# Kernel optimization log

Measured on AMD Instinct MI355X. Metric: run time of the kernel, lower is better.

Reference implementation:

```python
import jax, jax.numpy as jnp
import numpy as np

N = 50000
E = 800000
D = 64
EPS_BN = 1e-5
EPS_NORM = 1e-12


def _bn_train(x, gamma, beta):
    # BatchNorm1d in training mode: batch stats over axis 0, biased variance
    mu = jnp.mean(x, axis=0, keepdims=True)
    var = jnp.mean((x - mu) ** 2, axis=0, keepdims=True)
    return (x - mu) / jnp.sqrt(var + EPS_BN) * gamma + beta


def setup_inputs() -> dict:
    key = jax.random.key(0)
    ks = jax.random.split(key, 16)
    s = 1.0 / np.sqrt(D)
    s2 = 1.0 / np.sqrt(2 * D)
    return {
        "h": jax.random.normal(ks[0], (N, D), jnp.float32),
        "e": jax.random.normal(ks[1], (E, D), jnp.float32),
        "src": jax.random.randint(ks[2], (E,), 0, N, jnp.int32),
        "dst": jax.random.randint(ks[3], (E,), 0, N, jnp.int32),
        "A_W": jax.random.uniform(ks[4], (D, D), jnp.float32, -s, s),
        "A_b": jax.random.uniform(ks[5], (D,), jnp.float32, -s, s),
        "B_W": jax.random.uniform(ks[6], (D, D), jnp.float32, -s, s),
        "B_b": jax.random.uniform(ks[7], (D,), jnp.float32, -s, s),
        "C_W": jax.random.uniform(ks[8], (D, D), jnp.float32, -s, s),
        "C_b": jax.random.uniform(ks[9], (D,), jnp.float32, -s, s),
        "W_apply": jax.random.uniform(ks[10], (2 * D, D), jnp.float32, -s2, s2),
        "b_apply": jax.random.uniform(ks[11], (D,), jnp.float32, -s2, s2),
        "gamma_h": jnp.ones((D,), jnp.float32),
        "beta_h": jnp.zeros((D,), jnp.float32),
        "gamma_e": jnp.ones((D,), jnp.float32),
        "beta_e": jnp.zeros((D,), jnp.float32),
    }


def reference(h, e, src, dst, A_W, A_b, B_W, B_b, C_W, C_b,
              W_apply, b_apply, gamma_h, beta_h, gamma_e, beta_e):
    h_in, e_in = h, e
    # dropout p=0 -> identity
    Ah = h @ A_W + A_b            # [N, D]
    Bh = h @ B_W + B_b            # [N, D]
    Ce = e @ C_W + C_b            # [E, D]

    # message: e_ij = Ce + Bh_src + Bh_dst ; gated message sigma(e_ij)*Ah_src
    e_ij = Ce + Bh[src] + Bh[dst]                 # [E, D]
    msg = jax.nn.relu(jax.nn.sigmoid(e_ij) * Ah[src])  # [E, D]

    # reduce: per-destination-node max over mailbox
    c = jax.ops.segment_max(msg, dst, num_segments=N)  # [N, D], -inf if empty
    deg = jax.ops.segment_sum(jnp.ones((E,), msg.dtype), dst, num_segments=N)
    c = jnp.where(deg[:, None] > 0, c, 0.0)

    # apply/update: concat -> linear -> L2 normalize -> activation
    bundle = jnp.concatenate([h, c], axis=1) @ W_apply + b_apply  # [N, D]
    norm = jnp.sqrt(jnp.sum(bundle * bundle, axis=1, keepdims=True))
    bundle = bundle / jnp.maximum(norm, EPS_NORM)
    h_new = jax.nn.relu(bundle)

    e_new = jax.nn.relu(e_ij)

    h_new = _bn_train(h_new, gamma_h, beta_h)
    e_new = _bn_train(e_new, gamma_e, beta_e)

    h_out = h_in + h_new
    e_out = e_in + e_new
    return (h_out, e_out)
```

## Files before the change

kernel.cpp:

```cpp
#include <hip/hip_runtime.h>

typedef __attribute__((ext_vector_type(8))) short short8;
typedef __attribute__((ext_vector_type(4))) float f32x4;
typedef __attribute__((ext_vector_type(4))) unsigned short u16x4;
typedef __attribute__((ext_vector_type(4))) unsigned int u32x4;

#define DEV static __device__ __forceinline__

constexpr int NN = 50000;
constexpr int NE = 800000;
constexpr int NT_N = NN / 16;
constexpr int NT_E = NE / 16;
constexpr float EPS_BN = 1e-5f;
constexpr float EPS_NORM = 1e-12f;

DEV unsigned short f2b(float f) {
  unsigned u = __float_as_uint(f);
  return (unsigned short)((u + 0x7FFFu + ((u >> 16) & 1u)) >> 16);
}
DEV float b2f(unsigned short s) { return __uint_as_float(((unsigned)s) << 16); }

DEV short8 load_a_frag(const float* __restrict__ base, int row, int kbase) {
  const f32x4* p = reinterpret_cast<const f32x4*>(base + row * 64 + kbase);
  f32x4 v0 = p[0], v1 = p[1];
  short8 a;
  a[0] = f2b(v0[0]); a[1] = f2b(v0[1]); a[2] = f2b(v0[2]); a[3] = f2b(v0[3]);
  a[4] = f2b(v1[0]); a[5] = f2b(v1[1]); a[6] = f2b(v1[2]); a[7] = f2b(v1[3]);
  return a;
}

DEV short8 load_w_frag(const float* __restrict__ W, int kbase, int c0, int lane) {
  int kr = kbase + ((lane >> 4) << 3);
  int cc = c0 + (lane & 15);
  short8 b;
#pragma unroll
  for (int j = 0; j < 8; ++j) b[j] = f2b(W[(kr + j) * 64 + cc]);
  return b;
}

DEV f32x4 mfma16(short8 a, short8 b, f32x4 c) {
  return __builtin_amdgcn_mfma_f32_16x16x32_bf16(a, b, c, 0, 0, 0);
}

__global__ void k_init(u32x4* __restrict__ cbuf4, float* __restrict__ stats) {
  int i = blockIdx.x * 256 + threadIdx.x;
  if (i < NN * 16) {
    u32x4 z = {0u, 0u, 0u, 0u};
    cbuf4[i] = z;
  }
  if (i < 256) stats[i] = 0.0f;
}

__global__ void __launch_bounds__(256) k_node_lin(
    const float* __restrict__ h, const float* __restrict__ AW,
    const float* __restrict__ Ab, const float* __restrict__ BW,
    const float* __restrict__ Bb, float* __restrict__ Ah,
    float* __restrict__ Bh) {
  int lane = threadIdx.x & 63, warp = threadIdx.x >> 6;
  int tile = blockIdx.x * 4 + warp;
  if (tile >= NT_N) return;

  short8 wa[4][2], wb[4][2];
  float ab[4], bb[4];
#pragma unroll
  for (int t = 0; t < 4; ++t) {
#pragma unroll
    for (int kk = 0; kk < 2; ++kk) {
      wa[t][kk] = load_w_frag(AW, kk * 32, t * 16, lane);
      wb[t][kk] = load_w_frag(BW, kk * 32, t * 16, lane);
    }
    ab[t] = Ab[t * 16 + (lane & 15)];
    bb[t] = Bb[t * 16 + (lane & 15)];
  }

  int row0 = tile * 16;
  int ar = row0 + (lane & 15), kb = (lane >> 4) * 8;
  short8 a0 = load_a_frag(h, ar, kb);
  short8 a1 = load_a_frag(h, ar, 32 + kb);

  f32x4 zero = {0.f, 0.f, 0.f, 0.f};
  f32x4 accA[4], accB[4];
#pragma unroll
  for (int t = 0; t < 4; ++t) {
    accA[t] = mfma16(a0, wa[t][0], zero);
    accA[t] = mfma16(a1, wa[t][1], accA[t]);
    accB[t] = mfma16(a0, wb[t][0], zero);
    accB[t] = mfma16(a1, wb[t][1], accB[t]);
  }
#pragma unroll
  for (int t = 0; t < 4; ++t)
#pragma unroll
    for (int q = 0; q < 4; ++q) {
      int row = row0 + (lane >> 4) * 4 + q;
      int col = t * 16 + (lane & 15);
      Ah[row * 64 + col] = accA[t][q] + ab[t];
      Bh[row * 64 + col] = accB[t][q] + bb[t];
    }
}

__global__ void __launch_bounds__(256) k_edge(
    const float* __restrict__ e, const int* __restrict__ src,
    const int* __restrict__ dst, const float* __restrict__ CW,
    const float* __restrict__ Cb, const float* __restrict__ Ah,
    const float* __restrict__ Bh, unsigned* __restrict__ cbuf,
    float* __restrict__ gsum, float* __restrict__ gsq,
    float* __restrict__ stage_f32, unsigned short* __restrict__ stage_b16,
    int use_b16) {
  __shared__ float ssum[64], ssq[64];
  int lane = threadIdx.x & 63, warp = threadIdx.x >> 6;

  short8 cw[4][2];
  float cb[4];
#pragma unroll
  for (int t = 0; t < 4; ++t) {
#pragma unroll
    for (int kk = 0; kk < 2; ++kk) cw[t][kk] = load_w_frag(CW, kk * 32, t * 16, lane);
    cb[t] = Cb[t * 16 + (lane & 15)];
  }

  float es[4] = {0.f, 0.f, 0.f, 0.f}, eq[4] = {0.f, 0.f, 0.f, 0.f};
  f32x4 zero = {0.f, 0.f, 0.f, 0.f};
  int stride = gridDim.x * 4;

  for (int tile = blockIdx.x * 4 + warp; tile < NT_E; tile += stride) {
    int e0 = tile * 16;
    int ar = e0 + (lane & 15), kb = (lane >> 4) * 8;
    short8 a0 = load_a_frag(e, ar, kb);
    short8 a1 = load_a_frag(e, ar, 32 + kb);

    f32x4 acc[4];
#pragma unroll
    for (int t = 0; t < 4; ++t) {
      acc[t] = mfma16(a0, cw[t][0], zero);
      acc[t] = mfma16(a1, cw[t][1], acc[t]);
    }

#pragma unroll
    for (int q = 0; q < 4; ++q) {
      int er = e0 + (lane >> 4) * 4 + q;
      int s = src[er], d = dst[er];
#pragma unroll
      for (int t = 0; t < 4; ++t) {
        int col = t * 16 + (lane & 15);
        float eij = acc[t][q] + cb[t] + Bh[s * 64 + col] + Bh[d * 64 + col];
        float sg = __fdividef(1.0f, 1.0f + __expf(-eij));
        float m = sg * Ah[s * 64 + col];
        m = (m > 0.0f) ? m : 0.0f;
        atomicMax(&cbuf[d * 64 + col], __float_as_uint(m));
        float re = (eij > 0.0f) ? eij : 0.0f;
        if (use_b16) stage_b16[er * 64 + col] = f2b(re);
        else         stage_f32[er * 64 + col] = re;
        es[t] += re;
        eq[t] += re * re;
      }
    }
  }

  if (threadIdx.x < 64) { ssum[threadIdx.x] = 0.f; ssq[threadIdx.x] = 0.f; }
  __syncthreads();
#pragma unroll
  for (int t = 0; t < 4; ++t) {
    int col = t * 16 + (lane & 15);
    atomicAdd(&ssum[col], es[t]);
    atomicAdd(&ssq[col], eq[t]);
  }
  __syncthreads();
  if (threadIdx.x < 64) {
    atomicAdd(&gsum[threadIdx.x], ssum[threadIdx.x]);
    atomicAdd(&gsq[threadIdx.x], ssq[threadIdx.x]);
  }
}

__global__ void __launch_bounds__(256) k_apply(
    const float* __restrict__ h, const float* __restrict__ cbuf_f,
    const float* __restrict__ Wap, const float* __restrict__ bap,
    float* __restrict__ stage_h, float* __restrict__ gsum,
    float* __restrict__ gsq) {
  __shared__ float ssum[64], ssq[64];
  int lane = threadIdx.x & 63, warp = threadIdx.x >> 6;
  int tile = blockIdx.x * 4 + warp;

  float hs[4] = {0.f, 0.f, 0.f, 0.f}, hq[4] = {0.f, 0.f, 0.f, 0.f};

  if (tile < NT_N) {
    short8 w[4][4];
    float ba[4];
#pragma unroll
    for (int t = 0; t < 4; ++t) {
#pragma unroll
      for (int kk = 0; kk < 4; ++kk) w[t][kk] = load_w_frag(Wap, kk * 32, t * 16, lane);
      ba[t] = bap[t * 16 + (lane & 15)];
    }

    int row0 = tile * 16;
    int ar = row0 + (lane & 15), kb = (lane >> 4) * 8;
    short8 a0 = load_a_frag(h, ar, kb);
    short8 a1 = load_a_frag(h, ar, 32 + kb);
    short8 a2 = load_a_frag(cbuf_f, ar, kb);
    short8 a3 = load_a_frag(cbuf_f, ar, 32 + kb);

    f32x4 zero = {0.f, 0.f, 0.f, 0.f};
    f32x4 acc[4];
#pragma unroll
    for (int t = 0; t < 4; ++t) {
      acc[t] = mfma16(a0, w[t][0], zero);
      acc[t] = mfma16(a1, w[t][1], acc[t]);
      acc[t] = mfma16(a2, w[t][2], acc[t]);
      acc[t] = mfma16(a3, w[t][3], acc[t]);
    }

    float v[4][4];
#pragma unroll
    for (int t = 0; t < 4; ++t)
#pragma unroll
      for (int q = 0; q < 4; ++q) v[t][q] = acc[t][q] + ba[t];

#pragma unroll
    for (int q = 0; q < 4; ++q) {
      float sq = v[0][q] * v[0][q] + v[1][q] * v[1][q] + v[2][q] * v[2][q] +
                 v[3][q] * v[3][q];
      sq += __shfl_xor(sq, 1);
      sq += __shfl_xor(sq, 2);
      sq += __shfl_xor(sq, 4);
      sq += __shfl_xor(sq, 8);
      float sc = __fdividef(1.0f, fmaxf(sqrtf(sq), EPS_NORM));
      int row = row0 + (lane >> 4) * 4 + q;
#pragma unroll
      for (int t = 0; t < 4; ++t) {
        float hn = v[t][q] * sc;
        hn = (hn > 0.0f) ? hn : 0.0f;
        stage_h[row * 64 + t * 16 + (lane & 15)] = hn;
        hs[t] += hn;
        hq[t] += hn * hn;
      }
    }
  }

  if (threadIdx.x < 64) { ssum[threadIdx.x] = 0.f; ssq[threadIdx.x] = 0.f; }
  __syncthreads();
#pragma unroll
  for (int t = 0; t < 4; ++t) {
    int col = t * 16 + (lane & 15);
    atomicAdd(&ssum[col], hs[t]);
    atomicAdd(&ssq[col], hq[t]);
  }
  __syncthreads();
  if (threadIdx.x < 64) {
    atomicAdd(&gsum[threadIdx.x], ssum[threadIdx.x]);
    atomicAdd(&gsq[threadIdx.x], ssq[threadIdx.x]);
  }
}

__global__ void k_stats(const float* __restrict__ sum_e, const float* __restrict__ sq_e,
                        const float* __restrict__ sum_h, const float* __restrict__ sq_h,
                        const float* __restrict__ gamma_e, const float* __restrict__ beta_e,
                        const float* __restrict__ gamma_h, const float* __restrict__ beta_h,
                        float* __restrict__ se, float* __restrict__ oe,
                        float* __restrict__ sh, float* __restrict__ oh) {
  int j = threadIdx.x;
  if (j < 64) {
    float mu = sum_e[j] / (float)NE;
    float var = fmaxf(sq_e[j] / (float)NE - mu * mu, 0.0f);
    float s = gamma_e[j] / sqrtf(var + EPS_BN);
    se[j] = s;
    oe[j] = beta_e[j] - mu * s;
    mu = sum_h[j] / (float)NN;
    var = fmaxf(sq_h[j] / (float)NN - mu * mu, 0.0f);
    s = gamma_h[j] / sqrtf(var + EPS_BN);
    sh[j] = s;
    oh[j] = beta_h[j] - mu * s;
  }
}

__global__ void __launch_bounds__(256) k_fin_h(const float* __restrict__ h,
                                               const float* __restrict__ sh,
                                               const float* __restrict__ oh,
                                               float* __restrict__ outh) {
  int i = (blockIdx.x * 256 + threadIdx.x) * 4;
  if (i >= NN * 64) return;
  f32x4 x = *reinterpret_cast<const f32x4*>(outh + i);
  f32x4 hv = *reinterpret_cast<const f32x4*>(h + i);
  int c0 = i & 63;
  f32x4 r;
#pragma unroll
  for (int j = 0; j < 4; ++j) r[j] = hv[j] + x[j] * sh[c0 + j] + oh[c0 + j];
  *reinterpret_cast<f32x4*>(outh + i) = r;
}

__global__ void __launch_bounds__(256) k_fin_e(const float* __restrict__ e,
                                               const float* __restrict__ se,
                                               const float* __restrict__ oe,
                                               const unsigned short* __restrict__ stb,
                                               int use_b16,
                                               float* __restrict__ oute) {
  int i = (blockIdx.x * 256 + threadIdx.x) * 4;
  if (i >= NE * 64) return;
  f32x4 x;
  if (use_b16) {
    u16x4 u = *reinterpret_cast<const u16x4*>(stb + i);
    x[0] = b2f(u[0]); x[1] = b2f(u[1]); x[2] = b2f(u[2]); x[3] = b2f(u[3]);
  } else {
    x = *reinterpret_cast<const f32x4*>(oute + i);
  }
  f32x4 ev = *reinterpret_cast<const f32x4*>(e + i);
  int c0 = i & 63;
  f32x4 r;
#pragma unroll
  for (int j = 0; j < 4; ++j) r[j] = ev[j] + x[j] * se[c0 + j] + oe[c0 + j];
  *reinterpret_cast<f32x4*>(oute + i) = r;
}

extern "C" void kernel_launch(void* const* d_in, const int* in_sizes, int n_in,
                              void* d_out, int out_size, void* d_ws, size_t ws_size,
                              hipStream_t stream) {
  (void)in_sizes; (void)n_in; (void)out_size;
  const float* h   = (const float*)d_in[0];
  const float* e   = (const float*)d_in[1];
  const int*   src = (const int*)d_in[2];
  const int*   dst = (const int*)d_in[3];
  const float* AW  = (const float*)d_in[4];
  const float* Ab  = (const float*)d_in[5];
  const float* BW  = (const float*)d_in[6];
  const float* Bb  = (const float*)d_in[7];
  const float* CW  = (const float*)d_in[8];
  const float* Cb  = (const float*)d_in[9];
  const float* Wap = (const float*)d_in[10];
  const float* bap = (const float*)d_in[11];
  const float* gamma_h = (const float*)d_in[12];
  const float* beta_h  = (const float*)d_in[13];
  const float* gamma_e = (const float*)d_in[14];
  const float* beta_e  = (const float*)d_in[15];

  float* ws = (float*)d_ws;
  float* Ah = ws;
  float* Bh = ws + 3200000;
  unsigned* cbuf = (unsigned*)(ws + 6400000);
  float* stats = ws + 9600000;
  float* sum_e = stats;
  float* sq_e  = stats + 64;
  float* sum_h = stats + 128;
  float* sq_h  = stats + 192;
  float* se    = stats + 256;
  float* oe    = stats + 320;
  float* sh    = stats + 384;
  float* oh    = stats + 448;

  size_t base_bytes = (size_t)(9600000 + 512) * 4;
  int use_b16 = (ws_size >= base_bytes + (size_t)NE * 64 * 2) ? 1 : 0;
  unsigned short* stage_b16 = (unsigned short*)(ws + 9600512);

  float* outh = (float*)d_out;
  float* oute = outh + (size_t)NN * 64;
  float* stage_f32 = oute;

  k_init<<<3125, 256, 0, stream>>>((u32x4*)cbuf, stats);
  k_node_lin<<<(NT_N + 3) / 4, 256, 0, stream>>>(h, AW, Ab, BW, Bb, Ah, Bh);
  k_edge<<<2048, 256, 0, stream>>>(e, src, dst, CW, Cb, Ah, Bh, cbuf, sum_e,
                                   sq_e, stage_f32, stage_b16, use_b16);
  k_apply<<<(NT_N + 3) / 4, 256, 0, stream>>>(h, (const float*)cbuf, Wap, bap,
                                              outh, sum_h, sq_h);
  k_stats<<<1, 64, 0, stream>>>(sum_e, sq_e, sum_h, sq_h, gamma_e, beta_e,
                                gamma_h, beta_h, se, oe, sh, oh);
  k_fin_h<<<NN * 64 / 1024, 256, 0, stream>>>(h, sh, oh, outh);
  k_fin_e<<<NE * 64 / 1024, 256, 0, stream>>>(e, se, oe, stage_b16, use_b16, oute);
}
```

Before: 392.9 us.

## Replace atomicMax segment-max with CSR-sorted per-node gather reduction

Builds a CSR grouping of edges by destination on each call (degree count, scan, scatter into perm) and replaces the per-element global atomicMax in the edge kernel with a separate per-node warp reduction. The edge kernel now stages pre-ReLU e_ij, and the reduce kernel recomputes sigmoid times Ah[src] from it. The final edge kernel applies the ReLU instead. This removes 51M contended atomics and the cbuf zeroing. In exchange it adds several small launches, an extra gather pass over the staged e_ij (bf16 or f32), and a nondeterministic perm order that does not affect a max.

```diff
diff --git a/kernel.cpp b/kernel.cpp
--- a/kernel.cpp
+++ b/kernel.cpp
@@ -3,7 +3,6 @@
 typedef __attribute__((ext_vector_type(8))) short short8;
 typedef __attribute__((ext_vector_type(4))) float f32x4;
 typedef __attribute__((ext_vector_type(4))) unsigned short u16x4;
-typedef __attribute__((ext_vector_type(4))) unsigned int u32x4;
 
 #define DEV static __device__ __forceinline__
 
@@ -11,6 +10,7 @@
 constexpr int NE = 800000;
 constexpr int NT_N = NN / 16;
 constexpr int NT_E = NE / 16;
+constexpr int NB_SCAN = (NN + 255) / 256;
 constexpr float EPS_BN = 1e-5f;
 constexpr float EPS_NORM = 1e-12f;
 
@@ -42,13 +42,67 @@
   return __builtin_amdgcn_mfma_f32_16x16x32_bf16(a, b, c, 0, 0, 0);
 }
 
-__global__ void k_init(u32x4* __restrict__ cbuf4, float* __restrict__ stats) {
+__global__ void k_init(int* __restrict__ deg, float* __restrict__ stats) {
   int i = blockIdx.x * 256 + threadIdx.x;
-  if (i < NN * 16) {
-    u32x4 z = {0u, 0u, 0u, 0u};
-    cbuf4[i] = z;
-  }
-  if (i < 256) stats[i] = 0.0f;
+  if (i < NN) deg[i] = 0;
+  if (i < 512) stats[i] = 0.0f;
+}
+
+__global__ void k_deg(const int* __restrict__ dst, int* __restrict__ deg) {
+  int i = blockIdx.x * 256 + threadIdx.x;
+  if (i < NE) atomicAdd(&deg[dst[i]], 1);
+}
+
+__global__ void k_scan_local(const int* __restrict__ deg, int* __restrict__ off,
+                             int* __restrict__ bsum) {
+  __shared__ int sh[256];
+  int t = threadIdx.x;
+  int i = blockIdx.x * 256 + t;
+  int v = (i < NN) ? deg[i] : 0;
+  sh[t] = v;
+  __syncthreads();
+  for (int s = 1; s < 256; s <<= 1) {
+    int u = (t >= s) ? sh[t - s] : 0;
+    __syncthreads();
+    sh[t] += u;
+    __syncthreads();
+  }
+  if (i < NN) off[i] = sh[t] - v;
+  if (t == 255) bsum[blockIdx.x] = sh[255];
+}
+
+__global__ void k_scan_base(const int* __restrict__ bsum, int* __restrict__ bbase) {
+  __shared__ int sh[256];
+  int t = threadIdx.x;
+  int v = (t < NB_SCAN) ? bsum[t] : 0;
+  sh[t] = v;
+  __syncthreads();
+  for (int s = 1; s < 256; s <<= 1) {
+    int u = (t >= s) ? sh[t - s] : 0;
+    __syncthreads();
+    sh[t] += u;
+    __syncthreads();
+  }
+  if (t < NB_SCAN) bbase[t] = sh[t] - v;
+}
+
+__global__ void k_scan_fix(const int* __restrict__ bbase, int* __restrict__ off,
+                           int* __restrict__ cursor) {
+  int i = blockIdx.x * 256 + threadIdx.x;
+  if (i < NN) {
+    int o = off[i] + bbase[blockIdx.x];
+    off[i] = o;
+    cursor[i] = o;
+  }
+}
+
+__global__ void k_scatter(const int* __restrict__ dst, int* __restrict__ cursor,
+                          int* __restrict__ perm) {
+  int i = blockIdx.x * 256 + threadIdx.x;
+  if (i < NE) {
+    int p = atomicAdd(&cursor[dst[i]], 1);
+    perm[p] = i;
+  }
 }
 
 __global__ void __launch_bounds__(256) k_node_lin(
@@ -101,8 +155,7 @@
 __global__ void __launch_bounds__(256) k_edge(
     const float* __restrict__ e, const int* __restrict__ src,
     const int* __restrict__ dst, const float* __restrict__ CW,
-    const float* __restrict__ Cb, const float* __restrict__ Ah,
-    const float* __restrict__ Bh, unsigned* __restrict__ cbuf,
+    const float* __restrict__ Cb, const float* __restrict__ Bh,
     float* __restrict__ gsum, float* __restrict__ gsq,
     float* __restrict__ stage_f32, unsigned short* __restrict__ stage_b16,
     int use_b16) {
@@ -143,13 +196,9 @@
       for (int t = 0; t < 4; ++t) {
         int col = t * 16 + (lane & 15);
         float eij = acc[t][q] + cb[t] + Bh[s * 64 + col] + Bh[d * 64 + col];
-        float sg = __fdividef(1.0f, 1.0f + __expf(-eij));
-        float m = sg * Ah[s * 64 + col];
-        m = (m > 0.0f) ? m : 0.0f;
-        atomicMax(&cbuf[d * 64 + col], __float_as_uint(m));
+        if (use_b16) stage_b16[er * 64 + col] = f2b(eij);
+        else         stage_f32[er * 64 + col] = eij;
         float re = (eij > 0.0f) ? eij : 0.0f;
-        if (use_b16) stage_b16[er * 64 + col] = f2b(re);
-        else         stage_f32[er * 64 + col] = re;
         es[t] += re;
         eq[t] += re * re;
       }
@@ -169,6 +218,36 @@
     atomicAdd(&gsum[threadIdx.x], ssum[threadIdx.x]);
     atomicAdd(&gsq[threadIdx.x], ssq[threadIdx.x]);
   }
+}
+
+__global__ void __launch_bounds__(256) k_reduce(
+    const int* __restrict__ deg, const int* __restrict__ off,
+    const int* __restrict__ perm, const int* __restrict__ src,
+    const float* __restrict__ Ah, const unsigned short* __restrict__ st16,
+    const float* __restrict__ stF, int use_b16, float* __restrict__ cbuf) {
+  int lane = threadIdx.x & 63, warp = threadIdx.x >> 6;
+  int node = blockIdx.x * 4 + warp;
+  if (node >= NN) return;
+  int cnt = deg[node], base = off[node];
+  float m = 0.0f;
+  for (int b0 = 0; b0 < cnt; b0 += 64) {
+    int nb = min(64, cnt - b0);
+    int eid = 0, s = 0;
+    if (lane < nb) {
+      eid = perm[base + b0 + lane];
+      s = src[eid];
+    }
+#pragma unroll 4
+    for (int j = 0; j < nb; ++j) {
+      int ej = __shfl(eid, j);
+      int sj = __shfl(s, j);
+      float x = use_b16 ? b2f(st16[ej * 64 + lane]) : stF[ej * 64 + lane];
+      float sg = __fdividef(1.0f, 1.0f + __expf(-x));
+      float mm = sg * Ah[sj * 64 + lane];
+      m = fmaxf(m, (mm > 0.0f) ? mm : 0.0f);
+    }
+  }
+  cbuf[node * 64 + lane] = m;
 }
 
 __global__ void __launch_bounds__(256) k_apply(
@@ -306,7 +385,10 @@
   int c0 = i & 63;
   f32x4 r;
 #pragma unroll
-  for (int j = 0; j < 4; ++j) r[j] = ev[j] + x[j] * se[c0 + j] + oe[c0 + j];
+  for (int j = 0; j < 4; ++j) {
+    float rx = (x[j] > 0.0f) ? x[j] : 0.0f;
+    r[j] = ev[j] + rx * se[c0 + j] + oe[c0 + j];
+  }
   *reinterpret_cast<f32x4*>(oute + i) = r;
 }
 
@@ -332,10 +414,9 @@
   const float* beta_e  = (const float*)d_in[15];
 
   float* ws = (float*)d_ws;
-  float* Ah = ws;
-  float* Bh = ws + 3200000;
-  unsigned* cbuf = (unsigned*)(ws + 6400000);
-  float* stats = ws + 9600000;
+  float* Ah  = ws;
+  float* BhC = ws + 3200000;
+  float* stats = ws + 6400000;
   float* sum_e = stats;
   float* sq_e  = stats + 64;
   float* sum_h = stats + 128;
@@ -345,20 +426,34 @@
   float* sh    = stats + 384;
   float* oh    = stats + 448;
 
-  size_t base_bytes = (size_t)(9600000 + 512) * 4;
-  int use_b16 = (ws_size >= base_bytes + (size_t)NE * 64 * 2) ? 1 : 0;
-  unsigned short* stage_b16 = (unsigned short*)(ws + 9600512);
+  int* deg    = (int*)(ws + 6400512);
+  int* off    = deg + NN;
+  int* bsum   = off + NN;
+  int* bbase  = bsum + 256;
+  int* cursor = bbase + 256;
+  int* perm   = cursor + NN;
+  unsigned short* stage_b16 = (unsigned short*)(perm + NE);
+
+  size_t base_f32 = 6400512u + 3u * (size_t)NN + 512u + (size_t)NE;
+  int use_b16 = (ws_size >= base_f32 * 4 + (size_t)NE * 64 * 2) ? 1 : 0;
 
   float* outh = (float*)d_out;
   float* oute = outh + (size_t)NN * 64;
   float* stage_f32 = oute;
 
-  k_init<<<3125, 256, 0, stream>>>((u32x4*)cbuf, stats);
-  k_node_lin<<<(NT_N + 3) / 4, 256, 0, stream>>>(h, AW, Ab, BW, Bb, Ah, Bh);
-  k_edge<<<2048, 256, 0, stream>>>(e, src, dst, CW, Cb, Ah, Bh, cbuf, sum_e,
-                                   sq_e, stage_f32, stage_b16, use_b16);
-  k_apply<<<(NT_N + 3) / 4, 256, 0, stream>>>(h, (const float*)cbuf, Wap, bap,
-                                              outh, sum_h, sq_h);
+  k_init<<<NB_SCAN, 256, 0, stream>>>(deg, stats);
+  k_deg<<<(NE + 255) / 256, 256, 0, stream>>>(dst, deg);
+  k_scan_local<<<NB_SCAN, 256, 0, stream>>>(deg, off, bsum);
+  k_scan_base<<<1, 256, 0, stream>>>(bsum, bbase);
+  k_scan_fix<<<NB_SCAN, 256, 0, stream>>>(bbase, off, cursor);
+  k_scatter<<<(NE + 255) / 256, 256, 0, stream>>>(dst, cursor, perm);
+
+  k_node_lin<<<(NT_N + 3) / 4, 256, 0, stream>>>(h, AW, Ab, BW, Bb, Ah, BhC);
+  k_edge<<<2048, 256, 0, stream>>>(e, src, dst, CW, Cb, BhC, sum_e, sq_e,
+                                   stage_f32, stage_b16, use_b16);
+  k_reduce<<<(NN + 3) / 4, 256, 0, stream>>>(deg, off, perm, src, Ah,
+                                             stage_b16, stage_f32, use_b16, BhC);
+  k_apply<<<(NT_N + 3) / 4, 256, 0, stream>>>(h, BhC, Wap, bap, outh, sum_h, sq_h);
   k_stats<<<1, 64, 0, stream>>>(sum_e, sq_e, sum_h, sq_h, gamma_e, beta_e,
                                 gamma_h, beta_h, se, oe, sh, oh);
   k_fin_h<<<NN * 64 / 1024, 256, 0, stream>>>(h, sh, oh, outh);
```

Measured after the change: 526.3 us. 1.34x slower.

## Recompute edge features in final pass instead of staging, permute node layout, filter atomics

Applied to the files above, without the earlier changes.

The edge kernel no longer stores relu(e_ij) to a staging buffer. Instead the final edge pass recomputes e@C_W plus the gathered Bh terms and applies BatchNorm directly, trading a full write and read of E×64 values for extra MFMA work and gathers. Ah and Bh are now stored in a lane-permuted layout so each edge-row gather becomes one 16-byte vector load. The atomicMax is skipped when the current cbuf value is already larger, which cuts atomic traffic. k_init also drops its bounds check and zeroes 512 stats entries.

```diff
diff --git a/kernel.cpp b/kernel.cpp
--- a/kernel.cpp
+++ b/kernel.cpp
@@ -2,7 +2,6 @@
 
 typedef __attribute__((ext_vector_type(8))) short short8;
 typedef __attribute__((ext_vector_type(4))) float f32x4;
-typedef __attribute__((ext_vector_type(4))) unsigned short u16x4;
 typedef __attribute__((ext_vector_type(4))) unsigned int u32x4;
 
 #define DEV static __device__ __forceinline__
@@ -18,7 +17,6 @@
   unsigned u = __float_as_uint(f);
   return (unsigned short)((u + 0x7FFFu + ((u >> 16) & 1u)) >> 16);
 }
-DEV float b2f(unsigned short s) { return __uint_as_float(((unsigned)s) << 16); }
 
 DEV short8 load_a_frag(const float* __restrict__ base, int row, int kbase) {
   const f32x4* p = reinterpret_cast<const f32x4*>(base + row * 64 + kbase);
@@ -44,21 +42,20 @@
 
 __global__ void k_init(u32x4* __restrict__ cbuf4, float* __restrict__ stats) {
   int i = blockIdx.x * 256 + threadIdx.x;
-  if (i < NN * 16) {
-    u32x4 z = {0u, 0u, 0u, 0u};
-    cbuf4[i] = z;
-  }
-  if (i < 256) stats[i] = 0.0f;
+  u32x4 z = {0u, 0u, 0u, 0u};
+  cbuf4[i] = z;
+  if (i < 512) stats[i] = 0.0f;
 }
 
 __global__ void __launch_bounds__(256) k_node_lin(
     const float* __restrict__ h, const float* __restrict__ AW,
     const float* __restrict__ Ab, const float* __restrict__ BW,
-    const float* __restrict__ Bb, float* __restrict__ Ah,
-    float* __restrict__ Bh) {
+    const float* __restrict__ Bb, float* __restrict__ Ah_p,
+    float* __restrict__ Bh_p) {
   int lane = threadIdx.x & 63, warp = threadIdx.x >> 6;
   int tile = blockIdx.x * 4 + warp;
   if (tile >= NT_N) return;
+  int r = lane & 15;
 
   short8 wa[4][2], wb[4][2];
   float ab[4], bb[4];
@@ -69,12 +66,12 @@
       wa[t][kk] = load_w_frag(AW, kk * 32, t * 16, lane);
       wb[t][kk] = load_w_frag(BW, kk * 32, t * 16, lane);
     }
-    ab[t] = Ab[t * 16 + (lane & 15)];
-    bb[t] = Bb[t * 16 + (lane & 15)];
+    ab[t] = Ab[t * 16 + r];
+    bb[t] = Bb[t * 16 + r];
   }
 
   int row0 = tile * 16;
-  int ar = row0 + (lane & 15), kb = (lane >> 4) * 8;
+  int ar = row0 + r, kb = (lane >> 4) * 8;
   short8 a0 = load_a_frag(h, ar, kb);
   short8 a1 = load_a_frag(h, ar, 32 + kb);
 
@@ -88,26 +85,26 @@
     accB[t] = mfma16(a1, wb[t][1], accB[t]);
   }
 #pragma unroll
-  for (int t = 0; t < 4; ++t)
-#pragma unroll
-    for (int q = 0; q < 4; ++q) {
-      int row = row0 + (lane >> 4) * 4 + q;
-      int col = t * 16 + (lane & 15);
-      Ah[row * 64 + col] = accA[t][q] + ab[t];
-      Bh[row * 64 + col] = accB[t][q] + bb[t];
-    }
+  for (int q = 0; q < 4; ++q) {
+    int row = row0 + (lane >> 4) * 4 + q;
+    f32x4 va = {accA[0][q] + ab[0], accA[1][q] + ab[1], accA[2][q] + ab[2],
+                accA[3][q] + ab[3]};
+    f32x4 vb = {accB[0][q] + bb[0], accB[1][q] + bb[1], accB[2][q] + bb[2],
+                accB[3][q] + bb[3]};
+    *reinterpret_cast<f32x4*>(Ah_p + row * 64 + r * 4) = va;
+    *reinterpret_cast<f32x4*>(Bh_p + row * 64 + r * 4) = vb;
+  }
 }
 
 __global__ void __launch_bounds__(256) k_edge(
     const float* __restrict__ e, const int* __restrict__ src,
     const int* __restrict__ dst, const float* __restrict__ CW,
-    const float* __restrict__ Cb, const float* __restrict__ Ah,
-    const float* __restrict__ Bh, unsigned* __restrict__ cbuf,
-    float* __restrict__ gsum, float* __restrict__ gsq,
-    float* __restrict__ stage_f32, unsigned short* __restrict__ stage_b16,
-    int use_b16) {
+    const float* __restrict__ Cb, const float* __restrict__ Ah_p,
+    const float* __restrict__ Bh_p, unsigned* __restrict__ cbuf,
+    float* __restrict__ gsum, float* __restrict__ gsq) {
   __shared__ float ssum[64], ssq[64];
   int lane = threadIdx.x & 63, warp = threadIdx.x >> 6;
+  int r = lane & 15;
 
   short8 cw[4][2];
   float cb[4];
@@ -115,7 +112,7 @@
   for (int t = 0; t < 4; ++t) {
 #pragma unroll
     for (int kk = 0; kk < 2; ++kk) cw[t][kk] = load_w_frag(CW, kk * 32, t * 16, lane);
-    cb[t] = Cb[t * 16 + (lane & 15)];
+    cb[t] = Cb[t * 16 + r];
   }
 
   float es[4] = {0.f, 0.f, 0.f, 0.f}, eq[4] = {0.f, 0.f, 0.f, 0.f};
@@ -124,9 +121,9 @@
 
   for (int tile = blockIdx.x * 4 + warp; tile < NT_E; tile += stride) {
     int e0 = tile * 16;
-    int ar = e0 + (lane & 15), kb = (lane >> 4) * 8;
-    short8 a0 = load_a_frag(e, ar, kb);
-    short8 a1 = load_a_frag(e, ar, 32 + kb);
+    int kb = (lane >> 4) * 8;
+    short8 a0 = load_a_frag(e, e0 + r, kb);
+    short8 a1 = load_a_frag(e, e0 + r, 32 + kb);
 
     f32x4 acc[4];
 #pragma unroll
@@ -139,19 +136,21 @@
     for (int q = 0; q < 4; ++q) {
       int er = e0 + (lane >> 4) * 4 + q;
       int s = src[er], d = dst[er];
+      f32x4 bs = *reinterpret_cast<const f32x4*>(Bh_p + s * 64 + r * 4);
+      f32x4 bd = *reinterpret_cast<const f32x4*>(Bh_p + d * 64 + r * 4);
+      f32x4 av = *reinterpret_cast<const f32x4*>(Ah_p + s * 64 + r * 4);
 #pragma unroll
       for (int t = 0; t < 4; ++t) {
-        int col = t * 16 + (lane & 15);
-        float eij = acc[t][q] + cb[t] + Bh[s * 64 + col] + Bh[d * 64 + col];
-        float sg = __fdividef(1.0f, 1.0f + __expf(-eij));
-        float m = sg * Ah[s * 64 + col];
-        m = (m > 0.0f) ? m : 0.0f;
-        atomicMax(&cbuf[d * 64 + col], __float_as_uint(m));
+        float eij = acc[t][q] + cb[t] + bs[t] + bd[t];
         float re = (eij > 0.0f) ? eij : 0.0f;
-        if (use_b16) stage_b16[er * 64 + col] = f2b(re);
-        else         stage_f32[er * 64 + col] = re;
         es[t] += re;
         eq[t] += re * re;
+        float sg = __fdividef(1.0f, 1.0f + __expf(-eij));
+        float m = sg * av[t];
+        m = (m > 0.0f) ? m : 0.0f;
+        int idx = d * 64 + t * 16 + r;
+        float cur = __uint_as_float(cbuf[idx]);
+        if (m > cur) atomicMax(&cbuf[idx], __float_as_uint(m));
       }
     }
   }
@@ -160,7 +159,7 @@
   __syncthreads();
 #pragma unroll
   for (int t = 0; t < 4; ++t) {
-    int col = t * 16 + (lane & 15);
+    int col = t * 16 + r;
     atomicAdd(&ssum[col], es[t]);
     atomicAdd(&ssq[col], eq[t]);
   }
@@ -179,6 +178,7 @@
   __shared__ float ssum[64], ssq[64];
   int lane = threadIdx.x & 63, warp = threadIdx.x >> 6;
   int tile = blockIdx.x * 4 + warp;
+  int r = lane & 15;
 
   float hs[4] = {0.f, 0.f, 0.f, 0.f}, hq[4] = {0.f, 0.f, 0.f, 0.f};
 
@@ -189,11 +189,11 @@
     for (int t = 0; t < 4; ++t) {
 #pragma unroll
       for (int kk = 0; kk < 4; ++kk) w[t][kk] = load_w_frag(Wap, kk * 32, t * 16, lane);
-      ba[t] = bap[t * 16 + (lane & 15)];
+      ba[t] = bap[t * 16 + r];
     }
 
     int row0 = tile * 16;
-    int ar = row0 + (lane & 15), kb = (lane >> 4) * 8;
+    int ar = row0 + r, kb = (lane >> 4) * 8;
     short8 a0 = load_a_frag(h, ar, kb);
     short8 a1 = load_a_frag(h, ar, 32 + kb);
     short8 a2 = load_a_frag(cbuf_f, ar, kb);
@@ -229,7 +229,7 @@
       for (int t = 0; t < 4; ++t) {
         float hn = v[t][q] * sc;
         hn = (hn > 0.0f) ? hn : 0.0f;
-        stage_h[row * 64 + t * 16 + (lane & 15)] = hn;
+        stage_h[row * 64 + t * 16 + r] = hn;
         hs[t] += hn;
         hq[t] += hn * hn;
       }
@@ -240,7 +240,7 @@
   __syncthreads();
 #pragma unroll
   for (int t = 0; t < 4; ++t) {
-    int col = t * 16 + (lane & 15);
+    int col = t * 16 + r;
     atomicAdd(&ssum[col], hs[t]);
     atomicAdd(&ssq[col], hq[t]);
   }
@@ -281,39 +281,69 @@
   f32x4 x = *reinterpret_cast<const f32x4*>(outh + i);
   f32x4 hv = *reinterpret_cast<const f32x4*>(h + i);
   int c0 = i & 63;
-  f32x4 r;
-#pragma unroll
-  for (int j = 0; j < 4; ++j) r[j] = hv[j] + x[j] * sh[c0 + j] + oh[c0 + j];
-  *reinterpret_cast<f32x4*>(outh + i) = r;
-}
-
-__global__ void __launch_bounds__(256) k_fin_e(const float* __restrict__ e,
-                                               const float* __restrict__ se,
-                                               const float* __restrict__ oe,
-                                               const unsigned short* __restrict__ stb,
-                                               int use_b16,
-                                               float* __restrict__ oute) {
-  int i = (blockIdx.x * 256 + threadIdx.x) * 4;
-  if (i >= NE * 64) return;
-  f32x4 x;
-  if (use_b16) {
-    u16x4 u = *reinterpret_cast<const u16x4*>(stb + i);
-    x[0] = b2f(u[0]); x[1] = b2f(u[1]); x[2] = b2f(u[2]); x[3] = b2f(u[3]);
-  } else {
-    x = *reinterpret_cast<const f32x4*>(oute + i);
-  }
-  f32x4 ev = *reinterpret_cast<const f32x4*>(e + i);
-  int c0 = i & 63;
-  f32x4 r;
-#pragma unroll
-  for (int j = 0; j < 4; ++j) r[j] = ev[j] + x[j] * se[c0 + j] + oe[c0 + j];
-  *reinterpret_cast<f32x4*>(oute + i) = r;
+  f32x4 rr;
+#pragma unroll
+  for (int j = 0; j < 4; ++j) rr[j] = hv[j] + x[j] * sh[c0 + j] + oh[c0 + j];
+  *reinterpret_cast<f32x4*>(outh + i) = rr;
+}
+
+__global__ void __launch_bounds__(256) k_fin_e(
+    const float* __restrict__ e, const int* __restrict__ src,
+    const int* __restrict__ dst, const float* __restrict__ CW,
+    const float* __restrict__ Cb, const float* __restrict__ Bh_p,
+    const float* __restrict__ se, const float* __restrict__ oe,
+    float* __restrict__ oute) {
+  int lane = threadIdx.x & 63, warp = threadIdx.x >> 6;
+  int r = lane & 15;
+
+  short8 cw[4][2];
+  float cb[4], sev[4], oev[4];
+#pragma unroll
+  for (int t = 0; t < 4; ++t) {
+#pragma unroll
+    for (int kk = 0; kk < 2; ++kk) cw[t][kk] = load_w_frag(CW, kk * 32, t * 16, lane);
+    cb[t] = Cb[t * 16 + r];
+    sev[t] = se[t * 16 + r];
+    oev[t] = oe[t * 16 + r];
+  }
+
+  f32x4 zero = {0.f, 0.f, 0.f, 0.f};
+  int stride = gridDim.x * 4;
+
+  for (int tile = blockIdx.x * 4 + warp; tile < NT_E; tile += stride) {
+    int e0 = tile * 16;
+    int kb = (lane >> 4) * 8;
+    short8 a0 = load_a_frag(e, e0 + r, kb);
+    short8 a1 = load_a_frag(e, e0 + r, 32 + kb);
+
+    f32x4 acc[4];
+#pragma unroll
+    for (int t = 0; t < 4; ++t) {
+      acc[t] = mfma16(a0, cw[t][0], zero);
+      acc[t] = mfma16(a1, cw[t][1], acc[t]);
+    }
+
+#pragma unroll
+    for (int q = 0; q < 4; ++q) {
+      int er = e0 + (lane >> 4) * 4 + q;
+      int s = src[er], d = dst[er];
+      f32x4 bs = *reinterpret_cast<const f32x4*>(Bh_p + s * 64 + r * 4);
+      f32x4 bd = *reinterpret_cast<const f32x4*>(Bh_p + d * 64 + r * 4);
+#pragma unroll
+      for (int t = 0; t < 4; ++t) {
+        float eij = acc[t][q] + cb[t] + bs[t] + bd[t];
+        float re = (eij > 0.0f) ? eij : 0.0f;
+        int col = t * 16 + r;
+        oute[er * 64 + col] = e[er * 64 + col] + re * sev[t] + oev[t];
+      }
+    }
+  }
 }
 
 extern "C" void kernel_launch(void* const* d_in, const int* in_sizes, int n_in,
                               void* d_out, int out_size, void* d_ws, size_t ws_size,
                               hipStream_t stream) {
-  (void)in_sizes; (void)n_in; (void)out_size;
+  (void)in_sizes; (void)n_in; (void)out_size; (void)ws_size;
   const float* h   = (const float*)d_in[0];
   const float* e   = (const float*)d_in[1];
   const int*   src = (const int*)d_in[2];
@@ -332,8 +362,8 @@
   const float* beta_e  = (const float*)d_in[15];
 
   float* ws = (float*)d_ws;
-  float* Ah = ws;
-  float* Bh = ws + 3200000;
+  float* Ah_p = ws;
+  float* Bh_p = ws + 3200000;
   unsigned* cbuf = (unsigned*)(ws + 6400000);
   float* stats = ws + 9600000;
   float* sum_e = stats;
@@ -345,22 +375,17 @@
   float* sh    = stats + 384;
   float* oh    = stats + 448;
 
-  size_t base_bytes = (size_t)(9600000 + 512) * 4;
-  int use_b16 = (ws_size >= base_bytes + (size_t)NE * 64 * 2) ? 1 : 0;
-  unsigned short* stage_b16 = (unsigned short*)(ws + 9600512);
-
   float* outh = (float*)d_out;
   float* oute = outh + (size_t)NN * 64;
-  float* stage_f32 = oute;
 
   k_init<<<3125, 256, 0, stream>>>((u32x4*)cbuf, stats);
-  k_node_lin<<<(NT_N + 3) / 4, 256, 0, stream>>>(h, AW, Ab, BW, Bb, Ah, Bh);
-  k_edge<<<2048, 256, 0, stream>>>(e, src, dst, CW, Cb, Ah, Bh, cbuf, sum_e,
-                                   sq_e, stage_f32, stage_b16, use_b16);
+  k_node_lin<<<(NT_N + 3) / 4, 256, 0, stream>>>(h, AW, Ab, BW, Bb, Ah_p, Bh_p);
+  k_edge<<<2048, 256, 0, stream>>>(e, src, dst, CW, Cb, Ah_p, Bh_p, cbuf,
+                                   sum_e, sq_e);
   k_apply<<<(NT_N + 3) / 4, 256, 0, stream>>>(h, (const float*)cbuf, Wap, bap,
                                               outh, sum_h, sq_h);
   k_stats<<<1, 64, 0, stream>>>(sum_e, sq_e, sum_h, sq_h, gamma_e, beta_e,
                                 gamma_h, beta_h, se, oe, sh, oh);
   k_fin_h<<<NN * 64 / 1024, 256, 0, stream>>>(h, sh, oh, outh);
-  k_fin_e<<<NE * 64 / 1024, 256, 0, stream>>>(e, se, oe, stage_b16, use_b16, oute);
-}
+  k_fin_e<<<2048, 256, 0, stream>>>(e, src, dst, CW, Cb, Bh_p, se, oe, oute);
+}
```

Measured after the change: 604.7 us. +53.9%, slower.
